# Performance work log

Hardware: AMD Instinct MI355X
Metric: run time of the kernel (lower is better)

Reference implementation:

```python
import jax, jax.numpy as jnp
import numpy as np

N = 50000      # nodes
E = 800000     # edges (avg degree 16)
IN = 128       # in_dim0
H = 96         # hidden_dim
BN_EPS = 1e-5
PN_SCALE = 20.0


def setup_inputs() -> dict:
    key = jax.random.key(0)
    ks = jax.random.split(key, 12)
    s_in = 1.0 / np.sqrt(IN)
    s_h = 1.0 / np.sqrt(H)
    return {
        "x": jax.random.normal(ks[0], (N, IN), jnp.float32),
        "edge_index": jax.random.randint(ks[1], (2, E), 0, N, jnp.int32),
        # mlp0: Linear(in_dim0 -> hidden)
        "W0": jax.random.uniform(ks[2], (H, IN), jnp.float32, -s_in, s_in),
        "b0": jax.random.uniform(ks[3], (H,), jnp.float32, -s_in, s_in),
        # GIN MLP layer 1: Linear(hidden -> hidden) + BatchNorm
        "W1": jax.random.uniform(ks[4], (H, H), jnp.float32, -s_h, s_h),
        "b1": jax.random.uniform(ks[5], (H,), jnp.float32, -s_h, s_h),
        "gamma": jnp.ones((H,), jnp.float32),
        "beta": jnp.zeros((H,), jnp.float32),
        # GIN MLP layer 2: Linear(hidden -> hidden)
        "W2": jax.random.uniform(ks[6], (H, H), jnp.float32, -s_h, s_h),
        "b2": jax.random.uniform(ks[7], (H,), jnp.float32, -s_h, s_h),
    }


def reference(x, edge_index, W0, b0, W1, b1, gamma, beta, W2, b2):
    # h0 = mlp0(x)
    h0 = x @ W0.T + b0                                   # [N, H]

    # GINConv (eps=0): z_i = h0_i + sum_{j->i} h0_j
    src, dst = edge_index[0], edge_index[1]
    agg = jax.ops.segment_sum(h0[src], dst, num_segments=N)  # [N, H]
    z = h0 + agg

    # GIN MLP (layer_num=2): Linear -> BatchNorm(train) -> ReLU -> Linear
    h = z @ W1.T + b1
    mean = h.mean(axis=0)
    var = h.var(axis=0)                                  # biased, like torch BN
    h = (h - mean) * jax.lax.rsqrt(var + BN_EPS) * gamma + beta
    h = jax.nn.relu(h)
    l1 = h @ W2.T + b2                                   # [N, H]

    # PairNorm 'PN-SCS', scale=20
    col_mean = l1.mean(axis=0)
    rownorm = jnp.sqrt(1e-6 + jnp.sum(l1 * l1, axis=1, keepdims=True))
    l1 = PN_SCALE * l1 / rownorm - col_mean

    return (l1, h0)
```

## Files before the change

### kernel.cpp

```cpp
#include <hip/hip_runtime.h>

#define NN 50000
#define IN_DIM 128
#define HD 96
#define BN_EPS 1e-5f
#define PN_SCALE 20.0f
#define SCAN_NB 196

__device__ __forceinline__ float4 ld4(const float* p) { return *(const float4*)p; }
__device__ __forceinline__ float4 add4(float4 a, float4 b) {
    return make_float4(a.x + b.x, a.y + b.y, a.z + b.z, a.w + b.w);
}

__global__ void zero_kernel(float* stats, int* cnt) {
    int i = blockIdx.x * blockDim.x + threadIdx.x;
    if (i < 1024) stats[i] = 0.0f;
    int j = i - 1024;
    if (j >= 0 && j < NN) cnt[j] = 0;
}

template<int K, int MODE>
__global__ __launch_bounds__(256) void gemm_tiled(
    const float* A, const float* __restrict__ W, const float* __restrict__ bias,
    float* out, const float* __restrict__ scale, const float* __restrict__ shift,
    float* __restrict__ gsum, float* __restrict__ gsumsq,
    float* __restrict__ gcol, float* __restrict__ growss,
    const int* __restrict__ hist_dst, int* __restrict__ hist_cnt, int histE)
{
    constexpr int CK = 32;
    __shared__ float sh[64 * (CK + 1) + HD * (CK + 1)];
    float* As = sh;
    float* Ws = sh + 64 * (CK + 1);

    const int t  = threadIdx.x;

    if (MODE == 0) {
        int e0 = blockIdx.x * 1024 + t * 4;
#pragma unroll
        for (int i = 0; i < 4; ++i) {
            int e = e0 + i;
            if (e < histE) atomicAdd(&hist_cnt[hist_dst[e]], 1);
        }
    }

    const int tx = t & 15;
    const int ty = t >> 4;
    const int base = blockIdx.x * 64;

    float acc[4][6];
#pragma unroll
    for (int i = 0; i < 4; ++i)
#pragma unroll
        for (int j = 0; j < 6; ++j) acc[i][j] = 0.0f;

    for (int kc = 0; kc < K; kc += CK) {
#pragma unroll
        for (int it = 0; it < 2; ++it) {
            int q = t + it * 256;
            int r = q >> 3, c4 = q & 7;
            int row = base + r;
            float4 v = make_float4(0.f, 0.f, 0.f, 0.f);
            if (row < NN) v = ld4(A + (size_t)row * K + kc + c4 * 4);
            if (MODE == 2) {
                float4 sc = ld4(scale + kc + c4 * 4);
                float4 shf = ld4(shift + kc + c4 * 4);
                v.x = fmaxf(v.x * sc.x + shf.x, 0.f);
                v.y = fmaxf(v.y * sc.y + shf.y, 0.f);
                v.z = fmaxf(v.z * sc.z + shf.z, 0.f);
                v.w = fmaxf(v.w * sc.w + shf.w, 0.f);
            }
            float* d = As + r * (CK + 1) + c4 * 4;
            d[0] = v.x; d[1] = v.y; d[2] = v.z; d[3] = v.w;
        }
#pragma unroll
        for (int it = 0; it < 3; ++it) {
            int q = t + it * 256;
            int r = q >> 3, c4 = q & 7;
            float4 v = ld4(W + (size_t)r * K + kc + c4 * 4);
            float* d = Ws + r * (CK + 1) + c4 * 4;
            d[0] = v.x; d[1] = v.y; d[2] = v.z; d[3] = v.w;
        }
        __syncthreads();
#pragma unroll
        for (int kk = 0; kk < CK; ++kk) {
            float a[4], b[6];
#pragma unroll
            for (int i = 0; i < 4; ++i) a[i] = As[(ty * 4 + i) * (CK + 1) + kk];
#pragma unroll
            for (int j = 0; j < 6; ++j) b[j] = Ws[(tx * 6 + j) * (CK + 1) + kk];
#pragma unroll
            for (int i = 0; i < 4; ++i)
#pragma unroll
                for (int j = 0; j < 6; ++j) acc[i][j] += a[i] * b[j];
        }
        __syncthreads();
    }

    float cv[4][6];
#pragma unroll
    for (int j = 0; j < 6; ++j) {
        float bs = bias[tx * 6 + j];
#pragma unroll
        for (int i = 0; i < 4; ++i) cv[i][j] = acc[i][j] + bs;
    }
#pragma unroll
    for (int i = 0; i < 4; ++i) {
        int row = base + ty * 4 + i;
        if (row < NN) {
#pragma unroll
            for (int j = 0; j < 6; ++j)
                out[(size_t)row * HD + tx * 6 + j] = cv[i][j];
        }
    }

    if (MODE == 1) {
        float* rs_sum = sh;
        float* rs_sq  = sh + 1536;
        __syncthreads();
#pragma unroll
        for (int j = 0; j < 6; ++j) {
            float s = 0.f, q = 0.f;
#pragma unroll
            for (int i = 0; i < 4; ++i) {
                int row = base + ty * 4 + i;
                float v = (row < NN) ? cv[i][j] : 0.f;
                s += v; q += v * v;
            }
            rs_sum[ty * HD + tx * 6 + j] = s;
            rs_sq[ty * HD + tx * 6 + j]  = q;
        }
        __syncthreads();
        if (t < HD) {
            float S = 0.f, Q = 0.f;
#pragma unroll
            for (int r = 0; r < 16; ++r) { S += rs_sum[r * HD + t]; Q += rs_sq[r * HD + t]; }
            atomicAdd(&gsum[t], S);
            atomicAdd(&gsumsq[t], Q);
        }
    }

    if (MODE == 2) {
        float* rs_sum = sh;
        float* rr     = sh + 1536;
        __syncthreads();
#pragma unroll
        for (int j = 0; j < 6; ++j) {
            float s = 0.f;
#pragma unroll
            for (int i = 0; i < 4; ++i) {
                int row = base + ty * 4 + i;
                s += (row < NN) ? cv[i][j] : 0.f;
            }
            rs_sum[ty * HD + tx * 6 + j] = s;
        }
#pragma unroll
        for (int i = 0; i < 4; ++i) {
            float q = 0.f;
#pragma unroll
            for (int j = 0; j < 6; ++j) q += cv[i][j] * cv[i][j];
            rr[(ty * 4 + i) * 16 + tx] = q;
        }
        __syncthreads();
        if (t < HD) {
            float S = 0.f;
#pragma unroll
            for (int r = 0; r < 16; ++r) S += rs_sum[r * HD + t];
            atomicAdd(&gcol[t], S);
        }
        if (t < 64) {
            int row = base + t;
            if (row < NN) {
                float S = 0.f;
#pragma unroll
                for (int g = 0; g < 16; ++g) S += rr[t * 16 + g];
                growss[row] = S;
            }
        }
    }
}

__global__ __launch_bounds__(256) void scan_part1(const int* __restrict__ cnt,
                                                  int* __restrict__ bsum) {
    __shared__ int sh[256];
    int i = blockIdx.x * 256 + threadIdx.x;
    int t = threadIdx.x;
    sh[t] = (i < NN) ? cnt[i] : 0;
    __syncthreads();
    for (int off = 128; off > 0; off >>= 1) {
        if (t < off) sh[t] += sh[t + off];
        __syncthreads();
    }
    if (t == 0) bsum[blockIdx.x] = sh[0];
}

__global__ __launch_bounds__(256) void scan_part2(int* __restrict__ bsum) {
    __shared__ int sh[256];
    int t = threadIdx.x;
    int v = (t < SCAN_NB) ? bsum[t] : 0;
    sh[t] = v;
    __syncthreads();
    for (int off = 1; off < 256; off <<= 1) {
        int u = sh[t];
        if (t >= off) u += sh[t - off];
        __syncthreads();
        sh[t] = u;
        __syncthreads();
    }
    if (t < SCAN_NB) bsum[t] = sh[t] - v;
}

__global__ __launch_bounds__(256) void scan_part3(int* __restrict__ cnt,
                                                  const int* __restrict__ bsum,
                                                  int* __restrict__ rowptr) {
    __shared__ int sh[256];
    int i = blockIdx.x * 256 + threadIdx.x;
    int t = threadIdx.x;
    int v = (i < NN) ? cnt[i] : 0;
    sh[t] = v;
    __syncthreads();
    for (int off = 1; off < 256; off <<= 1) {
        int u = sh[t];
        if (t >= off) u += sh[t - off];
        __syncthreads();
        sh[t] = u;
        __syncthreads();
    }
    int excl = sh[t] - v + bsum[blockIdx.x];
    if (i < NN) { rowptr[i] = excl; cnt[i] = excl; }
    if (i == NN - 1) rowptr[NN] = excl + v;
}

__global__ __launch_bounds__(256) void fill_kernel(const int* __restrict__ ei,
                                                   int* __restrict__ cursor,
                                                   int* __restrict__ srcs, int E) {
    int t2 = blockIdx.x * 256 + threadIdx.x;
    int e0 = t2 * 2;
    int src[2], dst[2];
#pragma unroll
    for (int i = 0; i < 2; ++i) {
        int e = e0 + i;
        bool ok = e < E;
        dst[i] = ok ? ei[E + e] : -1;
        src[i] = ok ? ei[e] : 0;
    }
    for (int pass = 0; pass < 7; ++pass) {
#pragma unroll
        for (int i = 0; i < 2; ++i) {
            if (dst[i] >= 0 && (dst[i] >> 13) == pass) {
                int slot = atomicAdd(&cursor[dst[i]], 1);
                srcs[slot] = src[i];
            }
        }
    }
}

__global__ __launch_bounds__(192) void gather_kernel(
    const float* __restrict__ h0, const int* __restrict__ rowptr,
    const int* __restrict__ srcs, float* __restrict__ z)
{
    const int tid = threadIdx.x;
    const int rl  = tid / 24;
    const int c   = tid - rl * 24;
    const int row = blockIdx.x * 8 + rl;
    if (row >= NN) return;

    const int p0 = rowptr[row];
    const int p1 = rowptr[row + 1];

    float4 acc = ld4(h0 + (size_t)row * HD + c * 4);

    int p = p0;
    for (; p + 8 <= p1; p += 8) {
        int s0 = srcs[p + 0], s1 = srcs[p + 1], s2 = srcs[p + 2], s3 = srcs[p + 3];
        int s4 = srcs[p + 4], s5 = srcs[p + 5], s6 = srcs[p + 6], s7 = srcs[p + 7];
        float4 v0 = ld4(h0 + (size_t)s0 * HD + c * 4);
        float4 v1 = ld4(h0 + (size_t)s1 * HD + c * 4);
        float4 v2 = ld4(h0 + (size_t)s2 * HD + c * 4);
        float4 v3 = ld4(h0 + (size_t)s3 * HD + c * 4);
        float4 v4 = ld4(h0 + (size_t)s4 * HD + c * 4);
        float4 v5 = ld4(h0 + (size_t)s5 * HD + c * 4);
        float4 v6 = ld4(h0 + (size_t)s6 * HD + c * 4);
        float4 v7 = ld4(h0 + (size_t)s7 * HD + c * 4);
        acc = add4(acc, add4(add4(add4(v0, v1), add4(v2, v3)),
                             add4(add4(v4, v5), add4(v6, v7))));
    }
    for (; p + 4 <= p1; p += 4) {
        int s0 = srcs[p + 0], s1 = srcs[p + 1], s2 = srcs[p + 2], s3 = srcs[p + 3];
        float4 v0 = ld4(h0 + (size_t)s0 * HD + c * 4);
        float4 v1 = ld4(h0 + (size_t)s1 * HD + c * 4);
        float4 v2 = ld4(h0 + (size_t)s2 * HD + c * 4);
        float4 v3 = ld4(h0 + (size_t)s3 * HD + c * 4);
        acc = add4(acc, add4(add4(v0, v1), add4(v2, v3)));
    }
    for (; p < p1; ++p)
        acc = add4(acc, ld4(h0 + (size_t)srcs[p] * HD + c * 4));

    *(float4*)(z + (size_t)row * HD + c * 4) = acc;
}

__global__ void bn_finalize_kernel(const float* __restrict__ sum, const float* __restrict__ sumsq,
                                   const float* __restrict__ gamma, const float* __restrict__ beta,
                                   float* __restrict__ scale, float* __restrict__ shift)
{
    int f = threadIdx.x;
    if (f < HD) {
        float mean = sum[f] * (1.0f / NN);
        float var  = fmaxf(sumsq[f] * (1.0f / NN) - mean * mean, 0.0f);
        float rstd = rsqrtf(var + BN_EPS);
        float sc = rstd * gamma[f];
        scale[f] = sc;
        shift[f] = beta[f] - mean * sc;
    }
}

__global__ __launch_bounds__(256) void pn_kernel(float* l1, const float* __restrict__ colsum,
                                                 const float* __restrict__ rowss)
{
    int idx = blockIdx.x * 256 + threadIdx.x;
    if (idx >= NN * 24) return;
    int row = idx / 24;
    int q = idx - row * 24;
    float rs = rsqrtf(1e-6f + rowss[row]);
    float4 v = ld4(l1 + (size_t)idx * 4);
    float4 cm = ld4(colsum + q * 4);
    v.x = PN_SCALE * v.x * rs - cm.x * (1.0f / NN);
    v.y = PN_SCALE * v.y * rs - cm.y * (1.0f / NN);
    v.z = PN_SCALE * v.z * rs - cm.z * (1.0f / NN);
    v.w = PN_SCALE * v.w * rs - cm.w * (1.0f / NN);
    *(float4*)(l1 + (size_t)idx * 4) = v;
}

extern "C" void kernel_launch(void* const* d_in, const int* in_sizes, int n_in,
                              void* d_out, int out_size, void* d_ws, size_t ws_size,
                              hipStream_t stream) {
    const float* x     = (const float*)d_in[0];
    const int*   ei    = (const int*)d_in[1];
    const float* W0    = (const float*)d_in[2];
    const float* b0    = (const float*)d_in[3];
    const float* W1    = (const float*)d_in[4];
    const float* b1    = (const float*)d_in[5];
    const float* gamma = (const float*)d_in[6];
    const float* beta  = (const float*)d_in[7];
    const float* W2    = (const float*)d_in[8];
    const float* b2    = (const float*)d_in[9];

    float* out_l1 = (float*)d_out;
    float* out_h0 = out_l1 + (size_t)NN * HD;

    float* stats   = (float*)d_ws;
    float* s_sum   = stats;
    float* s_sumsq = stats + HD;
    float* s_col   = stats + 2 * HD;
    float* s_scale = stats + 288;
    float* s_shift = stats + 384;
    float* rowss = stats + 1024;
    int* cnt    = (int*)(rowss + NN);
    int* rowptr = cnt + NN;
    int* bsum   = rowptr + NN + 2;
    int* srcs   = bsum + 256;

    const int E = in_sizes[1] / 2;
    const int GB = (NN + 63) / 64;

    zero_kernel<<<(1024 + NN + 255) / 256, 256, 0, stream>>>(stats, cnt);
    gemm_tiled<IN_DIM, 0><<<GB, 256, 0, stream>>>(x, W0, b0, out_h0, nullptr, nullptr,
                                                  nullptr, nullptr, nullptr, nullptr,
                                                  ei + E, cnt, E);
    scan_part1<<<SCAN_NB, 256, 0, stream>>>(cnt, bsum);
    scan_part2<<<1, 256, 0, stream>>>(bsum);
    scan_part3<<<SCAN_NB, 256, 0, stream>>>(cnt, bsum, rowptr);
    fill_kernel<<<(E / 2 + 255) / 256, 256, 0, stream>>>(ei, cnt, srcs, E);
    gather_kernel<<<(NN + 7) / 8, 192, 0, stream>>>(out_h0, rowptr, srcs, out_l1);
    gemm_tiled<HD, 1><<<GB, 256, 0, stream>>>(out_l1, W1, b1, out_l1, nullptr, nullptr,
                                              s_sum, s_sumsq, nullptr, nullptr,
                                              nullptr, nullptr, 0);
    bn_finalize_kernel<<<1, 128, 0, stream>>>(s_sum, s_sumsq, gamma, beta, s_scale, s_shift);
    gemm_tiled<HD, 2><<<GB, 256, 0, stream>>>(out_l1, W2, b2, out_l1, s_scale, s_shift,
                                              nullptr, nullptr, s_col, rowss,
                                              nullptr, nullptr, 0);
    pn_kernel<<<(NN * 24 + 255) / 256, 256, 0, stream>>>(out_l1, s_col, rowss);
}
```

Baseline: 337.6 us.

## Replace SIMT tiled GEMMs with bf16 MFMA GEMMs and shuffle-based reductions

All three dense layers now run on matrix cores through 16x16x32 bf16 MFMA instructions. Each wave owns 16 rows, keeps its activations in registers with a one-step prefetch, and reads the weights after converting them to bf16 in LDS. The BatchNorm and PairNorm statistics now reduce with wave shuffles and a small LDS pass instead of large shared arrays, and the fused histogram uses vectorised int4 loads. The aim is to cut the FP32 FMA cost of the GEMMs. The trade is bf16 rounding of inputs and weights, which may push outputs closer to the tolerance limit.

Measured after the change: 306.3 us. 1.1x faster.

```diff
diff --git a/kernel.cpp b/kernel.cpp
--- a/kernel.cpp
+++ b/kernel.cpp
@@ -7,9 +7,24 @@
 #define PN_SCALE 20.0f
 #define SCAN_NB 196
 
+using bf16x8 = __attribute__((ext_vector_type(8))) short;
+using f32x4  = __attribute__((ext_vector_type(4))) float;
+
 __device__ __forceinline__ float4 ld4(const float* p) { return *(const float4*)p; }
 __device__ __forceinline__ float4 add4(float4 a, float4 b) {
     return make_float4(a.x + b.x, a.y + b.y, a.z + b.z, a.w + b.w);
+}
+
+__device__ __forceinline__ short bfr(float f) {
+    unsigned u = __float_as_uint(f);
+    unsigned r = u + 0x7fffu + ((u >> 16) & 1u);
+    return (short)(r >> 16);
+}
+__device__ __forceinline__ bf16x8 cvt8(float4 a, float4 b) {
+    bf16x8 r;
+    r[0] = bfr(a.x); r[1] = bfr(a.y); r[2] = bfr(a.z); r[3] = bfr(a.w);
+    r[4] = bfr(b.x); r[5] = bfr(b.y); r[6] = bfr(b.z); r[7] = bfr(b.w);
+    return r;
 }
 
 __global__ void zero_kernel(float* stats, int* cnt) {
@@ -20,161 +35,186 @@
 }
 
 template<int K, int MODE>
-__global__ __launch_bounds__(256) void gemm_tiled(
+__global__ __launch_bounds__(256) void gemm_mfma(
     const float* A, const float* __restrict__ W, const float* __restrict__ bias,
     float* out, const float* __restrict__ scale, const float* __restrict__ shift,
     float* __restrict__ gsum, float* __restrict__ gsumsq,
     float* __restrict__ gcol, float* __restrict__ growss,
-    const int* __restrict__ hist_dst, int* __restrict__ hist_cnt, int histE)
+    const int* __restrict__ ei, int* __restrict__ hist_cnt, int E)
 {
-    constexpr int CK = 32;
-    __shared__ float sh[64 * (CK + 1) + HD * (CK + 1)];
-    float* As = sh;
-    float* Ws = sh + 64 * (CK + 1);
-
-    const int t  = threadIdx.x;
+    constexpr int P   = K + 8;
+    constexpr int NS  = K / 32;
+    constexpr int KD4 = K / 4;
+    __shared__ short Wl[96 * P];
+
+    const int t    = threadIdx.x;
+    const int l    = t & 63;
+    const int w    = t >> 6;
+    const int l15  = l & 15;
+    const int lh   = l >> 4;
+    const int base = blockIdx.x * 64;
 
     if (MODE == 0) {
-        int e0 = blockIdx.x * 1024 + t * 4;
-#pragma unroll
-        for (int i = 0; i < 4; ++i) {
-            int e = e0 + i;
-            if (e < histE) atomicAdd(&hist_cnt[hist_dst[e]], 1);
-        }
-    }
-
-    const int tx = t & 15;
-    const int ty = t >> 4;
-    const int base = blockIdx.x * 64;
-
-    float acc[4][6];
-#pragma unroll
-    for (int i = 0; i < 4; ++i)
-#pragma unroll
-        for (int j = 0; j < 6; ++j) acc[i][j] = 0.0f;
-
-    for (int kc = 0; kc < K; kc += CK) {
-#pragma unroll
-        for (int it = 0; it < 2; ++it) {
-            int q = t + it * 256;
-            int r = q >> 3, c4 = q & 7;
-            int row = base + r;
-            float4 v = make_float4(0.f, 0.f, 0.f, 0.f);
-            if (row < NN) v = ld4(A + (size_t)row * K + kc + c4 * 4);
-            if (MODE == 2) {
-                float4 sc = ld4(scale + kc + c4 * 4);
-                float4 shf = ld4(shift + kc + c4 * 4);
-                v.x = fmaxf(v.x * sc.x + shf.x, 0.f);
-                v.y = fmaxf(v.y * sc.y + shf.y, 0.f);
-                v.z = fmaxf(v.z * sc.z + shf.z, 0.f);
-                v.w = fmaxf(v.w * sc.w + shf.w, 0.f);
+        int e0 = (blockIdx.x * 256 + t) * 4;
+        if (e0 + 4 <= E) {
+            int4 d4 = *(const int4*)(ei + E + e0);
+            atomicAdd(&hist_cnt[d4.x], 1); atomicAdd(&hist_cnt[d4.y], 1);
+            atomicAdd(&hist_cnt[d4.z], 1); atomicAdd(&hist_cnt[d4.w], 1);
+        } else {
+            for (int i = 0; i < 4; ++i) {
+                int e = e0 + i;
+                if (e < E) atomicAdd(&hist_cnt[ei[E + e]], 1);
             }
-            float* d = As + r * (CK + 1) + c4 * 4;
-            d[0] = v.x; d[1] = v.y; d[2] = v.z; d[3] = v.w;
-        }
-#pragma unroll
-        for (int it = 0; it < 3; ++it) {
-            int q = t + it * 256;
-            int r = q >> 3, c4 = q & 7;
-            float4 v = ld4(W + (size_t)r * K + kc + c4 * 4);
-            float* d = Ws + r * (CK + 1) + c4 * 4;
-            d[0] = v.x; d[1] = v.y; d[2] = v.z; d[3] = v.w;
-        }
-        __syncthreads();
-#pragma unroll
-        for (int kk = 0; kk < CK; ++kk) {
-            float a[4], b[6];
-#pragma unroll
-            for (int i = 0; i < 4; ++i) a[i] = As[(ty * 4 + i) * (CK + 1) + kk];
-#pragma unroll
-            for (int j = 0; j < 6; ++j) b[j] = Ws[(tx * 6 + j) * (CK + 1) + kk];
-#pragma unroll
-            for (int i = 0; i < 4; ++i)
-#pragma unroll
-                for (int j = 0; j < 6; ++j) acc[i][j] += a[i] * b[j];
-        }
-        __syncthreads();
-    }
-
-    float cv[4][6];
-#pragma unroll
-    for (int j = 0; j < 6; ++j) {
-        float bs = bias[tx * 6 + j];
-#pragma unroll
-        for (int i = 0; i < 4; ++i) cv[i][j] = acc[i][j] + bs;
-    }
-#pragma unroll
-    for (int i = 0; i < 4; ++i) {
-        int row = base + ty * 4 + i;
-        if (row < NN) {
-#pragma unroll
-            for (int j = 0; j < 6; ++j)
-                out[(size_t)row * HD + tx * 6 + j] = cv[i][j];
+        }
+    }
+
+    for (int c = t; c < 96 * KD4; c += 256) {
+        int row = c / KD4, kq = c - row * KD4;
+        float4 v = ld4(W + (size_t)row * K + kq * 4);
+        short4 s;
+        s.x = bfr(v.x); s.y = bfr(v.y); s.z = bfr(v.z); s.w = bfr(v.w);
+        *(short4*)(Wl + row * P + kq * 4) = s;
+    }
+    __syncthreads();
+
+    f32x4 acc[6];
+#pragma unroll
+    for (int n = 0; n < 6; ++n) acc[n] = (f32x4){0.f, 0.f, 0.f, 0.f};
+
+    const int  arow = base + w * 16 + l15;
+    const bool aok  = arow < NN;
+    const float* Ap = A + (size_t)arow * K + lh * 8;
+    const float4 Z4 = make_float4(0.f, 0.f, 0.f, 0.f);
+
+    float4 pa0 = aok ? ld4(Ap)     : Z4;
+    float4 pa1 = aok ? ld4(Ap + 4) : Z4;
+
+#pragma unroll
+    for (int s = 0; s < NS; ++s) {
+        float4 pb0 = Z4, pb1 = Z4;
+        if (s + 1 < NS && aok) {
+            pb0 = ld4(Ap + (s + 1) * 32);
+            pb1 = ld4(Ap + (s + 1) * 32 + 4);
+        }
+        float4 q0 = pa0, q1 = pa1;
+        if (MODE == 2) {
+            float4 sc0 = ld4(scale + s * 32 + lh * 8);
+            float4 sh0 = ld4(shift + s * 32 + lh * 8);
+            float4 sc1 = ld4(scale + s * 32 + lh * 8 + 4);
+            float4 sh1 = ld4(shift + s * 32 + lh * 8 + 4);
+            q0.x = fmaxf(q0.x * sc0.x + sh0.x, 0.f);
+            q0.y = fmaxf(q0.y * sc0.y + sh0.y, 0.f);
+            q0.z = fmaxf(q0.z * sc0.z + sh0.z, 0.f);
+            q0.w = fmaxf(q0.w * sc0.w + sh0.w, 0.f);
+            q1.x = fmaxf(q1.x * sc1.x + sh1.x, 0.f);
+            q1.y = fmaxf(q1.y * sc1.y + sh1.y, 0.f);
+            q1.z = fmaxf(q1.z * sc1.z + sh1.z, 0.f);
+            q1.w = fmaxf(q1.w * sc1.w + sh1.w, 0.f);
+        }
+        bf16x8 af = cvt8(q0, q1);
+        const short* wp = Wl + s * 32 + lh * 8;
+#pragma unroll
+        for (int n = 0; n < 6; ++n) {
+            bf16x8 bf = *(const bf16x8*)(wp + (n * 16 + l15) * P);
+            acc[n] = __builtin_amdgcn_mfma_f32_16x16x32_bf16(af, bf, acc[n], 0, 0, 0);
+        }
+        pa0 = pb0; pa1 = pb1;
+    }
+
+    float cv[6][4];
+#pragma unroll
+    for (int n = 0; n < 6; ++n) {
+        float b = bias[n * 16 + l15];
+#pragma unroll
+        for (int r = 0; r < 4; ++r) cv[n][r] = acc[n][r] + b;
+    }
+    int crow[4]; bool cok[4];
+#pragma unroll
+    for (int r = 0; r < 4; ++r) {
+        crow[r] = base + w * 16 + lh * 4 + r;
+        cok[r]  = crow[r] < NN;
+    }
+#pragma unroll
+    for (int r = 0; r < 4; ++r) {
+        if (cok[r]) {
+            float* o = out + (size_t)crow[r] * HD + l15;
+#pragma unroll
+            for (int n = 0; n < 6; ++n) o[n * 16] = cv[n][r];
         }
     }
 
     if (MODE == 1) {
-        float* rs_sum = sh;
-        float* rs_sq  = sh + 1536;
-        __syncthreads();
-#pragma unroll
-        for (int j = 0; j < 6; ++j) {
-            float s = 0.f, q = 0.f;
-#pragma unroll
-            for (int i = 0; i < 4; ++i) {
-                int row = base + ty * 4 + i;
-                float v = (row < NN) ? cv[i][j] : 0.f;
-                s += v; q += v * v;
+        float s[6], q[6];
+#pragma unroll
+        for (int n = 0; n < 6; ++n) {
+            s[n] = 0.f; q[n] = 0.f;
+#pragma unroll
+            for (int r = 0; r < 4; ++r) {
+                float v = cok[r] ? cv[n][r] : 0.f;
+                s[n] += v; q[n] += v * v;
             }
-            rs_sum[ty * HD + tx * 6 + j] = s;
-            rs_sq[ty * HD + tx * 6 + j]  = q;
+        }
+#pragma unroll
+        for (int n = 0; n < 6; ++n) {
+            s[n] += __shfl_xor(s[n], 16); s[n] += __shfl_xor(s[n], 32);
+            q[n] += __shfl_xor(q[n], 16); q[n] += __shfl_xor(q[n], 32);
+        }
+        __syncthreads();
+        float* red0 = (float*)Wl;
+        float* red1 = red0 + 384;
+        if (lh == 0) {
+#pragma unroll
+            for (int n = 0; n < 6; ++n) {
+                red0[w * 96 + n * 16 + l15] = s[n];
+                red1[w * 96 + n * 16 + l15] = q[n];
+            }
         }
         __syncthreads();
         if (t < HD) {
-            float S = 0.f, Q = 0.f;
-#pragma unroll
-            for (int r = 0; r < 16; ++r) { S += rs_sum[r * HD + t]; Q += rs_sq[r * HD + t]; }
+            float S = red0[t] + red0[96 + t] + red0[192 + t] + red0[288 + t];
+            float Q = red1[t] + red1[96 + t] + red1[192 + t] + red1[288 + t];
             atomicAdd(&gsum[t], S);
             atomicAdd(&gsumsq[t], Q);
         }
     }
 
     if (MODE == 2) {
-        float* rs_sum = sh;
-        float* rr     = sh + 1536;
-        __syncthreads();
-#pragma unroll
-        for (int j = 0; j < 6; ++j) {
-            float s = 0.f;
-#pragma unroll
-            for (int i = 0; i < 4; ++i) {
-                int row = base + ty * 4 + i;
-                s += (row < NN) ? cv[i][j] : 0.f;
-            }
-            rs_sum[ty * HD + tx * 6 + j] = s;
-        }
-#pragma unroll
-        for (int i = 0; i < 4; ++i) {
-            float q = 0.f;
-#pragma unroll
-            for (int j = 0; j < 6; ++j) q += cv[i][j] * cv[i][j];
-            rr[(ty * 4 + i) * 16 + tx] = q;
+        float s[6];
+#pragma unroll
+        for (int n = 0; n < 6; ++n) {
+            s[n] = 0.f;
+#pragma unroll
+            for (int r = 0; r < 4; ++r) s[n] += cok[r] ? cv[n][r] : 0.f;
+        }
+#pragma unroll
+        for (int n = 0; n < 6; ++n) {
+            s[n] += __shfl_xor(s[n], 16); s[n] += __shfl_xor(s[n], 32);
+        }
+        float rq[4];
+#pragma unroll
+        for (int r = 0; r < 4; ++r) {
+            float v = 0.f;
+#pragma unroll
+            for (int n = 0; n < 6; ++n) v = fmaf(cv[n][r], cv[n][r], v);
+            v += __shfl_xor(v, 1); v += __shfl_xor(v, 2);
+            v += __shfl_xor(v, 4); v += __shfl_xor(v, 8);
+            rq[r] = v;
+        }
+        __syncthreads();
+        float* red0 = (float*)Wl;
+        if (lh == 0) {
+#pragma unroll
+            for (int n = 0; n < 6; ++n) red0[w * 96 + n * 16 + l15] = s[n];
         }
         __syncthreads();
         if (t < HD) {
-            float S = 0.f;
-#pragma unroll
-            for (int r = 0; r < 16; ++r) S += rs_sum[r * HD + t];
+            float S = red0[t] + red0[96 + t] + red0[192 + t] + red0[288 + t];
             atomicAdd(&gcol[t], S);
         }
-        if (t < 64) {
-            int row = base + t;
-            if (row < NN) {
-                float S = 0.f;
-#pragma unroll
-                for (int g = 0; g < 16; ++g) S += rr[t * 16 + g];
-                growss[row] = S;
-            }
+        if (l15 == 0) {
+#pragma unroll
+            for (int r = 0; r < 4; ++r)
+                if (cok[r]) growss[crow[r]] = rq[r];
         }
     }
 }
@@ -363,20 +403,20 @@
     const int GB = (NN + 63) / 64;
 
     zero_kernel<<<(1024 + NN + 255) / 256, 256, 0, stream>>>(stats, cnt);
-    gemm_tiled<IN_DIM, 0><<<GB, 256, 0, stream>>>(x, W0, b0, out_h0, nullptr, nullptr,
-                                                  nullptr, nullptr, nullptr, nullptr,
-                                                  ei + E, cnt, E);
+    gemm_mfma<IN_DIM, 0><<<GB, 256, 0, stream>>>(x, W0, b0, out_h0, nullptr, nullptr,
+                                                 nullptr, nullptr, nullptr, nullptr,
+                                                 ei, cnt, E);
     scan_part1<<<SCAN_NB, 256, 0, stream>>>(cnt, bsum);
     scan_part2<<<1, 256, 0, stream>>>(bsum);
     scan_part3<<<SCAN_NB, 256, 0, stream>>>(cnt, bsum, rowptr);
     fill_kernel<<<(E / 2 + 255) / 256, 256, 0, stream>>>(ei, cnt, srcs, E);
     gather_kernel<<<(NN + 7) / 8, 192, 0, stream>>>(out_h0, rowptr, srcs, out_l1);
-    gemm_tiled<HD, 1><<<GB, 256, 0, stream>>>(out_l1, W1, b1, out_l1, nullptr, nullptr,
-                                              s_sum, s_sumsq, nullptr, nullptr,
-                                              nullptr, nullptr, 0);
+    gemm_mfma<HD, 1><<<GB, 256, 0, stream>>>(out_l1, W1, b1, out_l1, nullptr, nullptr,
+                                             s_sum, s_sumsq, nullptr, nullptr,
+                                             nullptr, nullptr, 0);
     bn_finalize_kernel<<<1, 128, 0, stream>>>(s_sum, s_sumsq, gamma, beta, s_scale, s_shift);
-    gemm_tiled<HD, 2><<<GB, 256, 0, stream>>>(out_l1, W2, b2, out_l1, s_scale, s_shift,
-                                              nullptr, nullptr, s_col, rowss,
-                                              nullptr, nullptr, 0);
+    gemm_mfma<HD, 2><<<GB, 256, 0, stream>>>(out_l1, W2, b2, out_l1, s_scale, s_shift,
+                                             nullptr, nullptr, s_col, rowss,
+                                             nullptr, nullptr, 0);
     pn_kernel<<<(NN * 24 + 255) / 256, 256, 0, stream>>>(out_l1, s_col, rowss);
 }
```
